# Kernel optimization log

Measured on AMD Instinct MI355X. Metric: run time of the kernel, lower is better.

Reference implementation:

```python
import jax, jax.numpy as jnp
import numpy as np

B, S, D, H, E, K = 8, 4096, 512, 2048, 8, 2


def setup_inputs() -> dict:
    key = jax.random.key(0)
    ks = jax.random.split(key, 8)
    def lin(k, shape, fan_in):
        return jax.random.normal(k, shape, jnp.float32) / np.sqrt(fan_in).astype(np.float32)
    return {
        "x": jax.random.normal(ks[0], (B, S, D), jnp.float32),
        "noise": jax.random.normal(ks[1], (B, S, E), jnp.float32),
        "Wg": lin(ks[2], (D, E), D), "bg": jnp.zeros((E,), jnp.float32),
        "Wn": lin(ks[3], (D, E), D), "bn": jnp.zeros((E,), jnp.float32),
        "W1": lin(ks[4], (E, D, H), D), "b1": jnp.zeros((E, H), jnp.float32),
        "W2": lin(ks[5], (E, H, D), H), "b2": jnp.zeros((E, D), jnp.float32),
    }


def reference(x, noise, Wg, bg, Wn, bn, W1, b1, W2, b2):
    # Noisy top-k router
    logits = x @ Wg + bg                                  # [B,S,E]
    noise_logits = x @ Wn + bn                            # [B,S,E]
    noisy = logits + noise * jax.nn.softplus(noise_logits)
    _, topi = jax.lax.top_k(noisy, K)                     # [B,S,K]
    # sparse softmax: -inf everywhere except the top-k expert slots
    sel = (topi[..., :, None] == jnp.arange(E)).any(axis=-2)  # [B,S,E] bool
    sparse = jnp.where(sel, noisy, -jnp.inf)
    gates = jax.nn.softmax(sparse, axis=-1)               # [B,S,E]; zeros off top-k
    # Combine: gates are exactly 0 for unselected experts, so the masked
    # gather-MLP-scatter loop equals a gate-weighted sum of expert MLPs.
    # (Expert dropout is identity in eval mode.)
    out = jnp.zeros_like(x)
    for e in range(E):  # small fixed expert count
        h = jax.nn.relu(x @ W1[e] + b1[e])                # [B,S,H]
        y = h @ W2[e] + b2[e]                             # [B,S,D]
        out = out + y * gates[..., e:e + 1]
    return out
```

## Files before the change

kernel.cpp:

```cpp
#include <hip/hip_runtime.h>

#define TT 32768
#define DD 512
#define HH 2048
#define EE 8
#define CAP 8192

typedef unsigned short u16;
typedef unsigned int u32;
typedef unsigned long long u64;
using short8  = __attribute__((ext_vector_type(8))) short;
using floatx4 = __attribute__((ext_vector_type(4))) float;

__device__ __forceinline__ u16 f2bf(float f) {
  unsigned u = __float_as_uint(f);
  u += 0x7FFFu + ((u >> 16) & 1u);
  return (u16)(u >> 16);
}

__device__ __forceinline__ void gl2lds16(const u16* g, char* l) {
  __builtin_amdgcn_global_load_lds(
      (const __attribute__((address_space(1))) u32*)(const void*)g,
      (__attribute__((address_space(3))) u32*)(void*)l, 16, 0, 0);
}

__global__ void transpose_bf16(const float* __restrict__ in, u16* __restrict__ out, int R, int C) {
  __shared__ float tile[32][33];
  int e = blockIdx.z;
  const float* src = in + (size_t)e * R * C;
  u16* dst = out + (size_t)e * R * C;
  int tx = threadIdx.x, ty = threadIdx.y;
  int c0 = blockIdx.x * 32, r0 = blockIdx.y * 32;
#pragma unroll
  for (int i = 0; i < 32; i += 8)
    tile[ty + i][tx] = src[(size_t)(r0 + ty + i) * C + c0 + tx];
  __syncthreads();
#pragma unroll
  for (int i = 0; i < 32; i += 8)
    dst[(size_t)(c0 + ty + i) * R + r0 + tx] = f2bf(tile[tx][ty + i]);
}

__global__ void router_topk(const float* __restrict__ x, const float* __restrict__ noise,
                            const float* __restrict__ Wg, const float* __restrict__ bg,
                            const float* __restrict__ Wn, const float* __restrict__ bn,
                            u16* __restrict__ xb, int* __restrict__ topk_i,
                            float* __restrict__ topk_g0, float* __restrict__ topk_g1) {
  const int t = (blockIdx.x * blockDim.x + threadIdx.x) >> 6;
  const int lane = threadIdx.x & 63;
  if (t >= TT) return;
  const float4* xr = (const float4*)(x + (size_t)t * DD) + lane * 2;
  float4 xa = xr[0], xbv = xr[1];
  float xv[8] = {xa.x, xa.y, xa.z, xa.w, xbv.x, xbv.y, xbv.z, xbv.w};
  {
    ushort4 o0, o1;
    o0.x = f2bf(xa.x); o0.y = f2bf(xa.y); o0.z = f2bf(xa.z); o0.w = f2bf(xa.w);
    o1.x = f2bf(xbv.x); o1.y = f2bf(xbv.y); o1.z = f2bf(xbv.z); o1.w = f2bf(xbv.w);
    ushort4* xo = (ushort4*)(xb + (size_t)t * DD) + lane * 2;
    xo[0] = o0; xo[1] = o1;
  }
  float pg[8], pn[8];
#pragma unroll
  for (int e = 0; e < 8; ++e) { pg[e] = 0.f; pn[e] = 0.f; }
  const float4* wg4 = (const float4*)(Wg + lane * 64);
  const float4* wn4 = (const float4*)(Wn + lane * 64);
#pragma unroll
  for (int j = 0; j < 8; ++j) {
    float xj = xv[j];
    float4 a = wg4[2 * j], b = wg4[2 * j + 1];
    pg[0] += xj * a.x; pg[1] += xj * a.y; pg[2] += xj * a.z; pg[3] += xj * a.w;
    pg[4] += xj * b.x; pg[5] += xj * b.y; pg[6] += xj * b.z; pg[7] += xj * b.w;
    a = wn4[2 * j]; b = wn4[2 * j + 1];
    pn[0] += xj * a.x; pn[1] += xj * a.y; pn[2] += xj * a.z; pn[3] += xj * a.w;
    pn[4] += xj * b.x; pn[5] += xj * b.y; pn[6] += xj * b.z; pn[7] += xj * b.w;
  }
#pragma unroll
  for (int off = 32; off; off >>= 1) {
#pragma unroll
    for (int e = 0; e < 8; ++e) {
      pg[e] += __shfl_xor(pg[e], off);
      pn[e] += __shfl_xor(pn[e], off);
    }
  }
  if (lane == 0) {
    float noisy[8];
#pragma unroll
    for (int e = 0; e < 8; ++e) {
      float nl = pn[e] + bn[e];
      float sp = (nl > 20.f) ? nl : log1pf(expf(nl));
      noisy[e] = pg[e] + bg[e] + noise[(size_t)t * EE + e] * sp;
    }
    int i0 = 0; float v0 = noisy[0];
#pragma unroll
    for (int e = 1; e < 8; ++e) if (noisy[e] > v0) { v0 = noisy[e]; i0 = e; }
    int i1 = -1; float v1 = -3.4e38f;
#pragma unroll
    for (int e = 0; e < 8; ++e) if (e != i0 && noisy[e] > v1) { v1 = noisy[e]; i1 = e; }
    float ed = expf(v1 - v0);
    float inv = 1.f / (1.f + ed);
    topk_i[t] = i0 | (i1 << 8);
    topk_g0[t] = inv;
    topk_g1[t] = ed * inv;
  }
}

__global__ void router_bin(const int* __restrict__ topk_i, const float* __restrict__ tg0,
                           const float* __restrict__ tg1,
                           int* __restrict__ countsA, int* __restrict__ countsB,
                           int* __restrict__ listsA, int* __restrict__ listsB,
                           float* __restrict__ gatesA, float* __restrict__ gatesB) {
  __shared__ int histA[EE], histB[EE], baseA[EE], baseB[EE];
  int t = blockIdx.x * 256 + threadIdx.x;
  if (threadIdx.x < EE) { histA[threadIdx.x] = 0; histB[threadIdx.x] = 0; }
  __syncthreads();
  int p = topk_i[t];
  int i0 = p & 255, i1 = p >> 8;
  int r0 = atomicAdd(&histA[i0], 1);
  int r1 = atomicAdd(&histB[i1], 1);
  __syncthreads();
  if (threadIdx.x < EE) {
    baseA[threadIdx.x] = atomicAdd(&countsA[threadIdx.x], histA[threadIdx.x]);
    baseB[threadIdx.x] = atomicAdd(&countsB[threadIdx.x], histB[threadIdx.x]);
  }
  __syncthreads();
  int s0 = baseA[i0] + r0, s1 = baseB[i1] + r1;
  if (s0 < CAP) { listsA[i0 * CAP + s0] = t; gatesA[i0 * CAP + s0] = tg0[t]; }
  if (s1 < CAP) { listsB[i1 * CAP + s1] = t; gatesB[i1 * CAP + s1] = tg1[t]; }
}

#define MS1 6
#define MS2 16
__global__ __launch_bounds__(256, 2)
void pass1_gemm(const u16* __restrict__ xb, const u16* __restrict__ w1t,
                const float* __restrict__ b1, const int* __restrict__ counts,
                const int* __restrict__ lists, u16* __restrict__ H) {
  __shared__ __align__(16) char lds[32768];
  char* ldsA = lds;
  char* ldsB = lds + 16384;
  const int e = blockIdx.x & 7;
  const int nt = (blockIdx.x >> 3) & 15;
  const int ms = blockIdx.x >> 7;
  int cnt = counts[e]; if (cnt > CAP) cnt = CAP;
  int eOff = 0;
#pragma unroll
  for (int j = 0; j < EE; ++j) {
    int cj = counts[j]; if (cj > CAP) cj = CAP;
    eOff += (j < e) ? cj : 0;
  }
  const int tid = threadIdx.x, lane = tid & 63, w = tid >> 6;
  const int col16 = lane & 15, quad = lane >> 4;
  const int hh = w & 1, mh = w >> 1;

  int rowi[4], kqi[4];
  const u16* wptr[4];
#pragma unroll
  for (int i = 0; i < 4; ++i) {
    int c = tid + i * 256;
    rowi[i] = c >> 3;
    kqi[i] = (c & 7) ^ (rowi[i] & 7);
    wptr[i] = w1t + (size_t)(e * HH + nt * 128 + rowi[i]) * DD + kqi[i] * 8;
  }

  for (int mtile = ms; mtile * 128 < cnt; mtile += MS1) {
    const u16* xptr[4];
#pragma unroll
    for (int i = 0; i < 4; ++i) {
      int idx = mtile * 128 + rowi[i];
      int tok = (idx < cnt) ? lists[e * CAP + idx] : 0;
      xptr[i] = xb + (size_t)tok * DD + kqi[i] * 8;
    }
    floatx4 acc[4][4];
#pragma unroll
    for (int a = 0; a < 4; ++a)
#pragma unroll
      for (int b = 0; b < 4; ++b) acc[a][b] = (floatx4){0.f, 0.f, 0.f, 0.f};

    for (int kc = 0; kc < DD / 64; ++kc) {
      __syncthreads();
#pragma unroll
      for (int i = 0; i < 4; ++i) {
        int off = (tid + i * 256) * 16;
        gl2lds16(wptr[i] + kc * 64, ldsA + off);
        gl2lds16(xptr[i] + kc * 64, ldsB + off);
      }
      __syncthreads();
#pragma unroll
      for (int ks = 0; ks < 2; ++ks) {
        short8 af[4], bf[4];
#pragma unroll
        for (int t4 = 0; t4 < 4; ++t4) {
          int rA = hh * 64 + t4 * 16 + col16;
          af[t4] = *(const short8*)(ldsA + (rA * 8 + ((ks * 4 + quad) ^ (rA & 7))) * 16);
          int rB = mh * 64 + t4 * 16 + col16;
          bf[t4] = *(const short8*)(ldsB + (rB * 8 + ((ks * 4 + quad) ^ (rB & 7))) * 16);
        }
#pragma unroll
        for (int ht = 0; ht < 4; ++ht)
#pragma unroll
          for (int mt = 0; mt < 4; ++mt)
            acc[ht][mt] = __builtin_amdgcn_mfma_f32_16x16x32_bf16(af[ht], bf[mt], acc[ht][mt], 0, 0, 0);
      }
    }
#pragma unroll
    for (int ht = 0; ht < 4; ++ht) {
      int hloc = nt * 128 + hh * 64 + ht * 16 + quad * 4;
      float b1v[4];
#pragma unroll
      for (int r = 0; r < 4; ++r) b1v[r] = b1[e * HH + hloc + r];
#pragma unroll
      for (int mt = 0; mt < 4; ++mt) {
        int gm = mtile * 128 + mh * 64 + mt * 16 + col16;
        if (gm < cnt) {
          u64 pk = 0;
#pragma unroll
          for (int r = 0; r < 4; ++r) {
            float f = fmaxf(acc[ht][mt][r] + b1v[r], 0.f);
            pk |= (u64)f2bf(f) << (16 * r);
          }
          *(u64*)(H + (size_t)(eOff + gm) * HH + hloc) = pk;
        }
      }
    }
  }
}

__global__ __launch_bounds__(256, 2)
void pass2_gemm(const u16* __restrict__ H, const u16* __restrict__ w2t,
                const float* __restrict__ b2, const int* __restrict__ counts,
                const int* __restrict__ lists, const float* __restrict__ gates,
                float* __restrict__ out, int rmw) {
  __shared__ __align__(16) char lds[32768];
  char* ldsA = lds;
  char* ldsB = lds + 16384;
  const int e = blockIdx.x & 7;
  const int nt = (blockIdx.x >> 3) & 3;
  const int ms = blockIdx.x >> 5;
  int cnt = counts[e]; if (cnt > CAP) cnt = CAP;
  int eOff = 0;
#pragma unroll
  for (int j = 0; j < EE; ++j) {
    int cj = counts[j]; if (cj > CAP) cj = CAP;
    eOff += (j < e) ? cj : 0;
  }
  const int tid = threadIdx.x, lane = tid & 63, w = tid >> 6;
  const int col16 = lane & 15, quad = lane >> 4;
  const int mh = w & 1, dh = w >> 1;

  int rowi[4], kqi[4];
  const u16* wptr[4];
#pragma unroll
  for (int i = 0; i < 4; ++i) {
    int c = tid + i * 256;
    rowi[i] = c >> 3;
    kqi[i] = (c & 7) ^ (rowi[i] & 7);
    wptr[i] = w2t + (size_t)(e * DD + nt * 128 + rowi[i]) * HH + kqi[i] * 8;
  }

  for (int mtile = ms; mtile * 128 < cnt; mtile += MS2) {
    const u16* hptr[4];
#pragma unroll
    for (int i = 0; i < 4; ++i)
      hptr[i] = H + (size_t)(eOff + mtile * 128 + rowi[i]) * HH + kqi[i] * 8;

    floatx4 acc[4][4];
#pragma unroll
    for (int a = 0; a < 4; ++a)
#pragma unroll
      for (int b = 0; b < 4; ++b) acc[a][b] = (floatx4){0.f, 0.f, 0.f, 0.f};

    for (int kc = 0; kc < HH / 64; ++kc) {
      __syncthreads();
#pragma unroll
      for (int i = 0; i < 4; ++i) {
        int off = (tid + i * 256) * 16;
        gl2lds16(hptr[i] + kc * 64, ldsA + off);
        gl2lds16(wptr[i] + kc * 64, ldsB + off);
      }
      __syncthreads();
#pragma unroll
      for (int ks = 0; ks < 2; ++ks) {
        short8 af[4], bf[4];
#pragma unroll
        for (int t4 = 0; t4 < 4; ++t4) {
          int rA = mh * 64 + t4 * 16 + col16;
          af[t4] = *(const short8*)(ldsA + (rA * 8 + ((ks * 4 + quad) ^ (rA & 7))) * 16);
          int rB = dh * 64 + t4 * 16 + col16;
          bf[t4] = *(const short8*)(ldsB + (rB * 8 + ((ks * 4 + quad) ^ (rB & 7))) * 16);
        }
#pragma unroll
        for (int mt = 0; mt < 4; ++mt)
#pragma unroll
          for (int dt = 0; dt < 4; ++dt)
            acc[mt][dt] = __builtin_amdgcn_mfma_f32_16x16x32_bf16(af[mt], bf[dt], acc[mt][dt], 0, 0, 0);
      }
    }
    float b2v[4];
#pragma unroll
    for (int dt = 0; dt < 4; ++dt)
      b2v[dt] = b2[e * DD + nt * 128 + dh * 64 + dt * 16 + col16];
#pragma unroll
    for (int mt = 0; mt < 4; ++mt) {
#pragma unroll
      for (int r = 0; r < 4; ++r) {
        int idx = mtile * 128 + mh * 64 + mt * 16 + quad * 4 + r;
        if (idx < cnt) {
          int tok = lists[e * CAP + idx];
          float g = gates[e * CAP + idx];
          float* orow = out + (size_t)tok * DD + nt * 128 + dh * 64;
          if (rmw) {
#pragma unroll
            for (int dt = 0; dt < 4; ++dt)
              orow[dt * 16 + col16] += g * (acc[mt][dt][r] + b2v[dt]);
          } else {
#pragma unroll
            for (int dt = 0; dt < 4; ++dt)
              orow[dt * 16 + col16] = g * (acc[mt][dt][r] + b2v[dt]);
          }
        }
      }
    }
  }
}

extern "C" void kernel_launch(void* const* d_in, const int* in_sizes, int n_in,
                              void* d_out, int out_size, void* d_ws, size_t ws_size,
                              hipStream_t stream) {
  const float* x     = (const float*)d_in[0];
  const float* noise = (const float*)d_in[1];
  const float* Wg    = (const float*)d_in[2];
  const float* bg    = (const float*)d_in[3];
  const float* Wn    = (const float*)d_in[4];
  const float* bn    = (const float*)d_in[5];
  const float* W1    = (const float*)d_in[6];
  const float* b1    = (const float*)d_in[7];
  const float* W2    = (const float*)d_in[8];
  const float* b2    = (const float*)d_in[9];
  float* out = (float*)d_out;
  char* ws = (char*)d_ws;

  u16*  w1t     = (u16*)(ws + 0x0000000);
  u16*  w2t     = (u16*)(ws + 0x1000000);
  u16*  xb      = (u16*)(ws + 0x2000000);
  int*  countsA = (int*)(ws + 0x4000000);
  int*  countsB = (int*)(ws + 0x4000020);
  int*  listsA  = (int*)(ws + 0x4010000);
  int*  listsB  = (int*)(ws + 0x4050000);
  float* gatesA = (float*)(ws + 0x4090000);
  float* gatesB = (float*)(ws + 0x40D0000);
  int*  topk_i  = (int*)(ws + 0x4110000);
  float* tg0    = (float*)(ws + 0x4130000);
  float* tg1    = (float*)(ws + 0x4150000);
  u16*  Hbuf    = (u16*)(ws + 0x4170000);
  (void)ws_size;

  hipMemsetAsync(countsA, 0, 64, stream);
  transpose_bf16<<<dim3(HH / 32, DD / 32, EE), dim3(32, 8), 0, stream>>>(W1, w1t, DD, HH);
  transpose_bf16<<<dim3(DD / 32, HH / 32, EE), dim3(32, 8), 0, stream>>>(W2, w2t, HH, DD);
  router_topk<<<TT / 4, 256, 0, stream>>>(x, noise, Wg, bg, Wn, bn, xb, topk_i, tg0, tg1);
  router_bin<<<TT / 256, 256, 0, stream>>>(topk_i, tg0, tg1, countsA, countsB,
                                           listsA, listsB, gatesA, gatesB);

  pass1_gemm<<<8 * 16 * MS1, 256, 0, stream>>>(xb, w1t, b1, countsA, listsA, Hbuf);
  pass2_gemm<<<8 * 4 * MS2, 256, 0, stream>>>(Hbuf, w2t, b2, countsA, listsA, gatesA, out, 0);
  pass1_gemm<<<8 * 16 * MS1, 256, 0, stream>>>(xb, w1t, b1, countsB, listsB, Hbuf);
  pass2_gemm<<<8 * 4 * MS2, 256, 0, stream>>>(Hbuf, w2t, b2, countsB, listsB, gatesB, out, 1);
}
```

Baseline: 767.2 us.

## Restructure router to stage tokens in LDS and raise GEMM split counts

```diff
diff --git a/kernel.cpp b/kernel.cpp
--- a/kernel.cpp
+++ b/kernel.cpp
@@ -40,66 +40,74 @@
     dst[(size_t)(c0 + ty + i) * R + r0 + tx] = f2bf(tile[tx][ty + i]);
 }
 
-__global__ void router_topk(const float* __restrict__ x, const float* __restrict__ noise,
-                            const float* __restrict__ Wg, const float* __restrict__ bg,
-                            const float* __restrict__ Wn, const float* __restrict__ bn,
-                            u16* __restrict__ xb, int* __restrict__ topk_i,
-                            float* __restrict__ topk_g0, float* __restrict__ topk_g1) {
-  const int t = (blockIdx.x * blockDim.x + threadIdx.x) >> 6;
-  const int lane = threadIdx.x & 63;
-  if (t >= TT) return;
-  const float4* xr = (const float4*)(x + (size_t)t * DD) + lane * 2;
-  float4 xa = xr[0], xbv = xr[1];
-  float xv[8] = {xa.x, xa.y, xa.z, xa.w, xbv.x, xbv.y, xbv.z, xbv.w};
-  {
-    ushort4 o0, o1;
-    o0.x = f2bf(xa.x); o0.y = f2bf(xa.y); o0.z = f2bf(xa.z); o0.w = f2bf(xa.w);
-    o1.x = f2bf(xbv.x); o1.y = f2bf(xbv.y); o1.z = f2bf(xbv.z); o1.w = f2bf(xbv.w);
-    ushort4* xo = (ushort4*)(xb + (size_t)t * DD) + lane * 2;
-    xo[0] = o0; xo[1] = o1;
-  }
-  float pg[8], pn[8];
-#pragma unroll
-  for (int e = 0; e < 8; ++e) { pg[e] = 0.f; pn[e] = 0.f; }
-  const float4* wg4 = (const float4*)(Wg + lane * 64);
-  const float4* wn4 = (const float4*)(Wn + lane * 64);
+__global__ void prep_router_w(const float* __restrict__ Wg, const float* __restrict__ Wn,
+                              float* __restrict__ wrt) {
+  int c = blockIdx.x;
+  int k = threadIdx.x;
+  wrt[c * 512 + k] = (c < 8) ? Wg[k * 8 + c] : Wn[k * 8 + (c - 8)];
+}
+
+__global__ __launch_bounds__(256)
+void router_topk(const float* __restrict__ x, const float* __restrict__ noise,
+                 const float* __restrict__ wrt, const float* __restrict__ bg,
+                 const float* __restrict__ bn,
+                 u16* __restrict__ xb, int* __restrict__ topk_i,
+                 float* __restrict__ tg0, float* __restrict__ tg1) {
+  __shared__ __align__(16) float xs[16 * 516];
+  const int tid = threadIdx.x;
+  const int blk = blockIdx.x;
+  const float4* xg = (const float4*)(x + (size_t)blk * 16 * DD);
+  ushort4* xo = (ushort4*)(xb + (size_t)blk * 16 * DD);
 #pragma unroll
   for (int j = 0; j < 8; ++j) {
-    float xj = xv[j];
-    float4 a = wg4[2 * j], b = wg4[2 * j + 1];
-    pg[0] += xj * a.x; pg[1] += xj * a.y; pg[2] += xj * a.z; pg[3] += xj * a.w;
-    pg[4] += xj * b.x; pg[5] += xj * b.y; pg[6] += xj * b.z; pg[7] += xj * b.w;
-    a = wn4[2 * j]; b = wn4[2 * j + 1];
-    pn[0] += xj * a.x; pn[1] += xj * a.y; pn[2] += xj * a.z; pn[3] += xj * a.w;
-    pn[4] += xj * b.x; pn[5] += xj * b.y; pn[6] += xj * b.z; pn[7] += xj * b.w;
-  }
-#pragma unroll
-  for (int off = 32; off; off >>= 1) {
-#pragma unroll
-    for (int e = 0; e < 8; ++e) {
-      pg[e] += __shfl_xor(pg[e], off);
-      pn[e] += __shfl_xor(pn[e], off);
-    }
-  }
-  if (lane == 0) {
-    float noisy[8];
-#pragma unroll
-    for (int e = 0; e < 8; ++e) {
-      float nl = pn[e] + bn[e];
-      float sp = (nl > 20.f) ? nl : log1pf(expf(nl));
-      noisy[e] = pg[e] + bg[e] + noise[(size_t)t * EE + e] * sp;
-    }
-    int i0 = 0; float v0 = noisy[0];
-#pragma unroll
-    for (int e = 1; e < 8; ++e) if (noisy[e] > v0) { v0 = noisy[e]; i0 = e; }
-    int i1 = -1; float v1 = -3.4e38f;
-#pragma unroll
-    for (int e = 0; e < 8; ++e) if (e != i0 && noisy[e] > v1) { v1 = noisy[e]; i1 = e; }
-    float ed = expf(v1 - v0);
+    int L = tid + j * 256;
+    int tk = L >> 7, j4 = L & 127;
+    float4 v = xg[L];
+    *(float4*)(xs + tk * 516 + j4 * 4) = v;
+    ushort4 o; o.x = f2bf(v.x); o.y = f2bf(v.y); o.z = f2bf(v.z); o.w = f2bf(v.w);
+    xo[L] = o;
+  }
+  __syncthreads();
+  const int tok = tid >> 4;
+  const int col = tid & 15;
+  const float4* wr = (const float4*)(wrt + col * 512);
+  const float4* xr = (const float4*)(xs + tok * 516);
+  float acc = 0.f;
+#pragma unroll 4
+  for (int k = 0; k < 128; ++k) {
+    float4 xv = xr[k];
+    float4 wv = wr[k];
+    acc += xv.x * wv.x + xv.y * wv.y + xv.z * wv.z + xv.w * wv.w;
+  }
+  const int t = blk * 16 + tok;
+  float other = __shfl_xor(acc, 8);
+  float noisy = -3.4e38f;
+  if (col < 8) {
+    float nl = other + bn[col];
+    float sp = (nl > 20.f) ? nl : log1pf(expf(nl));
+    noisy = acc + bg[col] + noise[(size_t)t * EE + col] * sp;
+  }
+  float v = noisy; int vi = col;
+#pragma unroll
+  for (int off = 1; off <= 4; off <<= 1) {
+    float ov = __shfl_xor(v, off);
+    int   oi = __shfl_xor(vi, off);
+    if (ov > v || (ov == v && oi < vi)) { v = ov; vi = oi; }
+  }
+  float v2 = (col == vi) ? -3.4e38f : noisy;
+  int vi2 = col;
+#pragma unroll
+  for (int off = 1; off <= 4; off <<= 1) {
+    float ov = __shfl_xor(v2, off);
+    int   oi = __shfl_xor(vi2, off);
+    if (ov > v2 || (ov == v2 && oi < vi2)) { v2 = ov; vi2 = oi; }
+  }
+  if (col == 0) {
+    float ed = expf(v2 - v);
     float inv = 1.f / (1.f + ed);
-    topk_i[t] = i0 | (i1 << 8);
-    topk_g0[t] = inv;
-    topk_g1[t] = ed * inv;
+    topk_i[t] = vi | (vi2 << 8);
+    tg0[t] = inv;
+    tg1[t] = ed * inv;
   }
 }
 
@@ -127,8 +135,8 @@
   if (s1 < CAP) { listsB[i1 * CAP + s1] = t; gatesB[i1 * CAP + s1] = tg1[t]; }
 }
 
-#define MS1 6
-#define MS2 16
+#define MS1 8
+#define MS2 32
 __global__ __launch_bounds__(256, 2)
 void pass1_gemm(const u16* __restrict__ xb, const u16* __restrict__ w1t,
                 const float* __restrict__ b1, const int* __restrict__ counts,
@@ -342,6 +350,7 @@
   u16*  xb      = (u16*)(ws + 0x2000000);
   int*  countsA = (int*)(ws + 0x4000000);
   int*  countsB = (int*)(ws + 0x4000020);
+  float* wrt    = (float*)(ws + 0x4002000);
   int*  listsA  = (int*)(ws + 0x4010000);
   int*  listsB  = (int*)(ws + 0x4050000);
   float* gatesA = (float*)(ws + 0x4090000);
@@ -353,9 +362,10 @@
   (void)ws_size;
 
   hipMemsetAsync(countsA, 0, 64, stream);
+  prep_router_w<<<16, 512, 0, stream>>>(Wg, Wn, wrt);
   transpose_bf16<<<dim3(HH / 32, DD / 32, EE), dim3(32, 8), 0, stream>>>(W1, w1t, DD, HH);
   transpose_bf16<<<dim3(DD / 32, HH / 32, EE), dim3(32, 8), 0, stream>>>(W2, w2t, HH, DD);
-  router_topk<<<TT / 4, 256, 0, stream>>>(x, noise, Wg, bg, Wn, bn, xb, topk_i, tg0, tg1);
+  router_topk<<<TT / 16, 256, 0, stream>>>(x, noise, wrt, bg, bn, xb, topk_i, tg0, tg1);
   router_bin<<<TT / 256, 256, 0, stream>>>(topk_i, tg0, tg1, countsA, countsB,
                                            listsA, listsB, gatesA, gatesB);
 
```

After: 761.9 us. Within noise of the previous version (-0.7%).
